# Optimization experiments

Measured on AMD Instinct MI355X. Metric: run time of the kernel, lower is better.

## Reference

```python
import jax, jax.numpy as jnp
import numpy as np

N = 100000
E = 1600000
IN_DIM, HID_DIM, OUT_DIM = 128, 64, 32


def setup_inputs() -> dict:
    key = jax.random.key(0)
    k1, k2, k3, k4, k5, k6 = jax.random.split(key, 6)
    x = jax.random.normal(k1, (N, IN_DIM), dtype=jnp.float32)
    edge_index = jax.random.randint(k2, (2, E), 0, N, dtype=jnp.int64)
    # Glorot-ish init for GCN weights
    W1 = jax.random.normal(k3, (IN_DIM, HID_DIM), dtype=jnp.float32) / np.sqrt(IN_DIM)
    b1 = jnp.zeros((HID_DIM,), dtype=jnp.float32)
    W2 = jax.random.normal(k4, (HID_DIM, OUT_DIM), dtype=jnp.float32) / np.sqrt(HID_DIM)
    b2 = jnp.zeros((OUT_DIM,), dtype=jnp.float32)
    return {"x": x, "edge_index": edge_index, "W1": W1, "b1": b1, "W2": W2, "b2": b2}


def _gcn_norm(edge_index, num_nodes):
    # add self loops, compute symmetric normalization coefficients
    loop = jnp.arange(num_nodes, dtype=edge_index.dtype)
    row = jnp.concatenate([edge_index[0], loop])  # source
    col = jnp.concatenate([edge_index[1], loop])  # target
    deg = jax.ops.segment_sum(jnp.ones_like(col, dtype=jnp.float32), col,
                              num_segments=num_nodes)
    dinv = jax.lax.rsqrt(deg)  # deg >= 1 due to self loops
    norm = dinv[row] * dinv[col]  # [E+N]
    return row, col, norm


def _gcn_conv(x, W, b, row, col, norm, num_nodes):
    h = x @ W                       # [N, out]
    msg = h[row] * norm[:, None]    # gather + scale  [E+N, out]
    out = jax.ops.segment_sum(msg, col, num_segments=num_nodes)  # scatter-add
    return out + b


def reference(x, edge_index, W1, b1, W2, b2):
    num_nodes = x.shape[0]
    row, col, norm = _gcn_norm(edge_index, num_nodes)
    h = _gcn_conv(x, W1, b1, row, col, norm, num_nodes)
    h = jax.nn.relu(h)
    # dropout(p=0.6) is identity in eval mode
    out = _gcn_conv(h, W2, b2, row, col, norm, num_nodes)
    return out
```

## Files before the change

### kernel.cpp

```cpp
#include <hip/hip_runtime.h>
#include <hip/hip_fp16.h>


#define NNODES 100000
#define NEDGES 1600000
#define IN_DIM 128
#define HID 64
#define OUTD 32

#define BKT_NODES 128
#define NBUK 782
#define BKT_CAP 3584
#define P1_BLOCKS 256
#define P1_CHUNK (NEDGES / P1_BLOCKS)


__global__ __launch_bounds__(256) void k_pass1(const int* __restrict__ row,
                                               const int* __restrict__ col,
                                               int* __restrict__ gcur,
                                               unsigned int* __restrict__ pairbuf) {
    __shared__ int lcnt[NBUK];
    __shared__ int lbase[NBUK];
    int t = threadIdx.x;
    int e0 = blockIdx.x * P1_CHUNK;
    int e1 = e0 + P1_CHUNK;
    for (int j = t; j < NBUK; j += 256) lcnt[j] = 0;
    __syncthreads();
    for (int e = e0 + t; e < e1; e += 256)
        atomicAdd(&lcnt[col[e] >> 7], 1);
    __syncthreads();
    for (int j = t; j < NBUK; j += 256) {
        int n = lcnt[j];
        lbase[j] = (n > 0) ? atomicAdd(&gcur[j], n) : 0;
    }
    __syncthreads();
    for (int j = t; j < NBUK; j += 256) lcnt[j] = 0;
    __syncthreads();
    for (int e = e0 + t; e < e1; e += 256) {
        int c = col[e];
        unsigned int pk = ((unsigned int)row[e] << 7) | (unsigned int)(c & 127);
        int b = c >> 7;
        int pos = lbase[b] + atomicAdd(&lcnt[b], 1);
        if (pos < BKT_CAP) pairbuf[(size_t)b * BKT_CAP + pos] = pk;
    }
}

__global__ __launch_bounds__(256) void k_pass2(const unsigned int* __restrict__ pairbuf,
                                               const int* __restrict__ gcur,
                                               int* __restrict__ ptr,
                                               float* __restrict__ dinv,
                                               int* __restrict__ adj) {
    __shared__ int ncnt[BKT_NODES];
    __shared__ int nsc[BKT_NODES];
    __shared__ int ncur[BKT_NODES];
    __shared__ int red[256];
    __shared__ int seg[BKT_CAP];
    int b = blockIdx.x;
    int t = threadIdx.x;

    int part = 0;
    for (int j = t; j < b; j += 256) part += gcur[j];
    red[t] = part;
    __syncthreads();
    for (int o = 128; o > 0; o >>= 1) {
        if (t < o) red[t] += red[t + o];
        __syncthreads();
    }
    int base = red[0];

    int c0 = b * BKT_NODES;
    int nb = NNODES - c0; if (nb > BKT_NODES) nb = BKT_NODES;
    int size = gcur[b]; if (size > BKT_CAP) size = BKT_CAP;
    const unsigned int* pp = pairbuf + (size_t)b * BKT_CAP;

    if (t < BKT_NODES) ncnt[t] = 0;
    __syncthreads();
    for (int k = t; k < size; k += 256)
        atomicAdd(&ncnt[pp[k] & 127u], 1);
    __syncthreads();
    int myv = (t < BKT_NODES) ? ncnt[t] : 0;
    if (t < BKT_NODES) nsc[t] = myv;
    __syncthreads();
    for (int off = 1; off < BKT_NODES; off <<= 1) {
        int u = 0;
        if (t < BKT_NODES && t >= off) u = nsc[t - off];
        __syncthreads();
        if (t < BKT_NODES) nsc[t] += u;
        __syncthreads();
    }
    if (t < BKT_NODES) {
        int excl = nsc[t] - myv;
        ncur[t] = excl;
        if (t < nb) {
            ptr[c0 + t] = base + excl;
            dinv[c0 + t] = rsqrtf((float)myv + 1.0f);
        }
    }
    if (b == NBUK - 1 && t == 0) ptr[NNODES] = NEDGES;
    __syncthreads();
    for (int k = t; k < size; k += 256) {
        unsigned int pk = pp[k];
        int pos = atomicAdd(&ncur[pk & 127u], 1);
        seg[pos] = (int)(pk >> 7);
    }
    __syncthreads();
    for (int k = t; k < size; k += 256) adj[base + k] = seg[k];
}


#define TILE 64
#define NT 16
__global__ __launch_bounds__(256) void k_gemm1(const float* __restrict__ x,
                                               const float* __restrict__ W1,
                                               const float* __restrict__ dinv,
                                               __half* __restrict__ g1) {
    __shared__ float shx[TILE][IN_DIM];
    int t = threadIdx.x;
    int nbase = blockIdx.x * TILE;

    const float4* xg = reinterpret_cast<const float4*>(x + (size_t)nbase * IN_DIM);
    float4* shx4 = reinterpret_cast<float4*>(&shx[0][0]);
    int lim = (NNODES - nbase) * (IN_DIM / 4);
    if (lim > TILE * (IN_DIM / 4)) lim = TILE * (IN_DIM / 4);
#pragma unroll
    for (int it = 0; it < 8; ++it) {
        int idx = t + it * 256;
        if (idx < lim) shx4[idx] = xg[idx];
    }
    __syncthreads();

    int w = t >> 6;
    int lane = t & 63;
    int n0 = w * NT;

    float acc[NT];
#pragma unroll
    for (int n = 0; n < NT; ++n) acc[n] = 0.0f;

    for (int kc = 0; kc < IN_DIM / 4; ++kc) {
        float w0 = W1[(kc * 4 + 0) * HID + lane];
        float w1 = W1[(kc * 4 + 1) * HID + lane];
        float w2 = W1[(kc * 4 + 2) * HID + lane];
        float w3 = W1[(kc * 4 + 3) * HID + lane];
#pragma unroll
        for (int n = 0; n < NT; ++n) {
            float4 xv = *reinterpret_cast<const float4*>(&shx[n0 + n][kc * 4]);
            acc[n] = fmaf(xv.x, w0, acc[n]);
            acc[n] = fmaf(xv.y, w1, acc[n]);
            acc[n] = fmaf(xv.z, w2, acc[n]);
            acc[n] = fmaf(xv.w, w3, acc[n]);
        }
    }
#pragma unroll
    for (int n = 0; n < NT; ++n) {
        int node = nbase + n0 + n;
        if (node < NNODES)
            g1[(unsigned)node * HID + lane] = __float2half(dinv[node] * acc[n]);
    }
}

__global__ __launch_bounds__(256) void k_agg1g2(const uint2* __restrict__ g1q,
                                                const int* __restrict__ ptr,
                                                const int* __restrict__ adj,
                                                const float* __restrict__ dinv,
                                                const float* __restrict__ b1,
                                                const float* __restrict__ W2,
                                                __half* __restrict__ g2,
                                                int ibase) {
    __shared__ float sh[4][HID];
    int t = blockIdx.x * blockDim.x + threadIdx.x;
    int i = ibase + (t >> 6);
    if (i >= NNODES) return;
    unsigned lane = threadIdx.x & 63;
    int w = threadIdx.x >> 6;
    unsigned q  = lane >> 4;
    unsigned hl = lane & 15;

    float4 acc = make_float4(0.f, 0.f, 0.f, 0.f);
    auto addrow = [&](unsigned n) {
        uint2 v = g1q[(n << 4) + hl];
        float2 fa = __half22float2(*reinterpret_cast<const __half2*>(&v.x));
        float2 fb = __half22float2(*reinterpret_cast<const __half2*>(&v.y));
        acc.x += fa.x; acc.y += fa.y; acc.z += fb.x; acc.w += fb.y;
    };

    if (q == 0) addrow((unsigned)i);
    int p0 = ptr[i], p1 = ptr[i + 1];
    int p = p0;
    for (; p + 16 <= p1; p += 16) {
        int n0 = adj[p + q];
        int n1 = adj[p + 4 + q];
        int n2 = adj[p + 8 + q];
        int n3 = adj[p + 12 + q];
        addrow((unsigned)n0);
        addrow((unsigned)n1);
        addrow((unsigned)n2);
        addrow((unsigned)n3);
    }
    for (; p + 4 <= p1; p += 4) {
        int n = adj[p + q];
        addrow((unsigned)n);
    }
    int rem = p1 - p;
    if ((int)q < rem) {
        int n = adj[p + q];
        addrow((unsigned)n);
    }
    acc.x += __shfl_xor(acc.x, 16); acc.y += __shfl_xor(acc.y, 16);
    acc.z += __shfl_xor(acc.z, 16); acc.w += __shfl_xor(acc.w, 16);
    acc.x += __shfl_xor(acc.x, 32); acc.y += __shfl_xor(acc.y, 32);
    acc.z += __shfl_xor(acc.z, 32); acc.w += __shfl_xor(acc.w, 32);

    float di = dinv[i];
    if (q == 0) {
        float4 bb = reinterpret_cast<const float4*>(b1)[hl];
        float4 h;
        h.x = fmaxf(fmaf(di, acc.x, bb.x), 0.f);
        h.y = fmaxf(fmaf(di, acc.y, bb.y), 0.f);
        h.z = fmaxf(fmaf(di, acc.z, bb.z), 0.f);
        h.w = fmaxf(fmaf(di, acc.w, bb.w), 0.f);
        *reinterpret_cast<float4*>(&sh[w][4 * hl]) = h;
    }

    unsigned j2 = lane & 31;
    unsigned half = lane >> 5;
    float mv = 0.0f;
#pragma unroll
    for (int j = 0; j < 32; ++j) {
        unsigned jj = half * 32 + j;
        mv = fmaf(sh[w][jj], W2[jj * OUTD + j2], mv);
    }
    mv += __shfl_xor(mv, 32);
    if (half == 0) g2[((unsigned)i << 5) + j2] = __float2half(di * mv);
}

__global__ __launch_bounds__(256) void k_agg2(const uint2* __restrict__ g2q,
                                              const int* __restrict__ ptr,
                                              const int* __restrict__ adj,
                                              const float* __restrict__ dinv,
                                              const float* __restrict__ b2,
                                              float4* __restrict__ out4) {
    int t = blockIdx.x * blockDim.x + threadIdx.x;
    int i = t >> 6;
    if (i >= NNODES) return;
    unsigned lane = threadIdx.x & 63;
    unsigned q  = lane >> 3;
    unsigned hl = lane & 7;

    float4 acc = make_float4(0.f, 0.f, 0.f, 0.f);
    auto addrow = [&](unsigned n) {
        uint2 v = g2q[(n << 3) + hl];
        float2 fa = __half22float2(*reinterpret_cast<const __half2*>(&v.x));
        float2 fb = __half22float2(*reinterpret_cast<const __half2*>(&v.y));
        acc.x += fa.x; acc.y += fa.y; acc.z += fb.x; acc.w += fb.y;
    };

    if (q == 0) addrow((unsigned)i);
    int p0 = ptr[i], p1 = ptr[i + 1];
    int p = p0;
    for (; p + 16 <= p1; p += 16) {
        int n0 = adj[p + q];
        int n1 = adj[p + 8 + q];
        addrow((unsigned)n0);
        addrow((unsigned)n1);
    }
    for (; p + 8 <= p1; p += 8) {
        int n = adj[p + q];
        addrow((unsigned)n);
    }
    int rem = p1 - p;
    if ((int)q < rem) {
        int n = adj[p + q];
        addrow((unsigned)n);
    }
    acc.x += __shfl_xor(acc.x, 8);  acc.y += __shfl_xor(acc.y, 8);
    acc.z += __shfl_xor(acc.z, 8);  acc.w += __shfl_xor(acc.w, 8);
    acc.x += __shfl_xor(acc.x, 16); acc.y += __shfl_xor(acc.y, 16);
    acc.z += __shfl_xor(acc.z, 16); acc.w += __shfl_xor(acc.w, 16);
    acc.x += __shfl_xor(acc.x, 32); acc.y += __shfl_xor(acc.y, 32);
    acc.z += __shfl_xor(acc.z, 32); acc.w += __shfl_xor(acc.w, 32);

    if (q == 0) {
        float di = dinv[i];
        float4 bb = reinterpret_cast<const float4*>(b2)[hl];
        out4[((unsigned)i << 3) + hl] =
            make_float4(fmaf(di, acc.x, bb.x), fmaf(di, acc.y, bb.y),
                        fmaf(di, acc.z, bb.z), fmaf(di, acc.w, bb.w));
    }
}

extern "C" void kernel_launch(void* const* d_in, const int* in_sizes, int n_in,
                              void* d_out, int out_size, void* d_ws, size_t ws_size,
                              hipStream_t stream) {
    const float* x  = (const float*)d_in[0];
    const int*   ei = (const int*)d_in[1];
    const float* W1 = (const float*)d_in[2];
    const float* b1 = (const float*)d_in[3];
    const float* W2 = (const float*)d_in[4];
    const float* b2 = (const float*)d_in[5];
    float4* out = (float4*)d_out;

    const int* row = ei;
    const int* col = ei + NEDGES;

    char* ws = (char*)d_ws;
    size_t off = 0;
    auto alloc = [&](size_t bytes) {
        void* p = ws + off;
        off = (off + bytes + 511) & ~(size_t)511;
        return p;
    };
    int*    gcur = (int*)   alloc((size_t)NBUK * 4);
    int*    ptr  = (int*)   alloc((size_t)(NNODES + 1) * 4);
    float*  dinv = (float*) alloc((size_t)NNODES * 4);
    int*    adj  = (int*)   alloc((size_t)NEDGES * 4);
    __half* g2   = (__half*)alloc((size_t)NNODES * OUTD * 2);
    size_t big = (size_t)NBUK * BKT_CAP * 4;
    size_t g1b = (size_t)NNODES * HID * 2;
    unsigned int* pairbuf = (unsigned int*)alloc(big > g1b ? big : g1b);
    __half* g1 = (__half*)pairbuf;

    const int B = 256;
    hipMemsetAsync(gcur, 0, (size_t)NBUK * 4, stream);
    k_pass1<<<P1_BLOCKS, 256, 0, stream>>>(row, col, gcur, pairbuf);
    k_pass2<<<NBUK, 256, 0, stream>>>(pairbuf, gcur, ptr, dinv, adj);

    {
        int nblk = (NNODES + TILE - 1) / TILE;
        k_gemm1<<<nblk, 256, 0, stream>>>(x, W1, dinv, g1);
    }
    {
        const int H0 = 50048;
        int nblk0 = H0 / 4;
        int nblk1 = (NNODES - H0 + 3) / 4;
        k_agg1g2<<<nblk0, B, 0, stream>>>(
            (const uint2*)g1, ptr, adj, dinv, b1, W2, g2, 0);
        k_agg1g2<<<nblk1, B, 0, stream>>>(
            (const uint2*)g1, ptr, adj, dinv, b1, W2, g2, H0);
    }
    {
        long long tot = (long long)NNODES * 64;
        k_agg2<<<(int)((tot + B - 1) / B), B, 0, stream>>>(
            (const uint2*)g2, ptr, adj, dinv, b2, out);
    }
}
```

Before: 286.9 us.

## Use fp16 MFMA for first GEMM and merge split aggregation launches

Replaces the fp32 FMA shared-memory GEMM for x@W1 with per-wave 16x16x32 fp16 MFMA instructions. A new one-block kernel pre-converts W1 to fp16 in MFMA fragment layout, and x rows are converted to fp16 in registers. The two half-range launches of the layer-1 aggregation are merged into a single launch. This lowers GEMM compute cost and launch overhead, but reduces the precision of the x@W1 inputs to fp16.

```diff
diff --git a/kernel.cpp b/kernel.cpp
--- a/kernel.cpp
+++ b/kernel.cpp
@@ -13,6 +13,9 @@
 #define BKT_CAP 3584
 #define P1_BLOCKS 256
 #define P1_CHUNK (NEDGES / P1_BLOCKS)
+
+typedef _Float16 f16x8 __attribute__((ext_vector_type(8)));
+typedef float f32x4 __attribute__((ext_vector_type(4)));
 
 
 __global__ __launch_bounds__(256) void k_pass1(const int* __restrict__ row,
@@ -108,54 +111,63 @@
 }
 
 
-#define TILE 64
-#define NT 16
+__global__ __launch_bounds__(256) void k_cvtW(const float* __restrict__ W1,
+                                              _Float16* __restrict__ W1h) {
+    int t = threadIdx.x;
+#pragma unroll
+    for (int it = 0; it < 4; ++it) {
+        int fl = t + it * 256;
+        int slot = fl >> 6;
+        int l = fl & 63;
+        int kk = slot >> 2, nt = slot & 3;
+        int kbase = kk * 32 + ((l >> 4) << 3);
+        int n = nt * 16 + (l & 15);
+        _Float16* dst = W1h + (size_t)fl * 8;
+#pragma unroll
+        for (int j = 0; j < 8; ++j)
+            dst[j] = (_Float16)W1[(kbase + j) * HID + n];
+    }
+}
+
 __global__ __launch_bounds__(256) void k_gemm1(const float* __restrict__ x,
-                                               const float* __restrict__ W1,
+                                               const f16x8* __restrict__ W1h,
                                                const float* __restrict__ dinv,
                                                __half* __restrict__ g1) {
-    __shared__ float shx[TILE][IN_DIM];
-    int t = threadIdx.x;
-    int nbase = blockIdx.x * TILE;
-
-    const float4* xg = reinterpret_cast<const float4*>(x + (size_t)nbase * IN_DIM);
-    float4* shx4 = reinterpret_cast<float4*>(&shx[0][0]);
-    int lim = (NNODES - nbase) * (IN_DIM / 4);
-    if (lim > TILE * (IN_DIM / 4)) lim = TILE * (IN_DIM / 4);
-#pragma unroll
-    for (int it = 0; it < 8; ++it) {
-        int idx = t + it * 256;
-        if (idx < lim) shx4[idx] = xg[idx];
-    }
-    __syncthreads();
-
-    int w = t >> 6;
-    int lane = t & 63;
-    int n0 = w * NT;
-
-    float acc[NT];
-#pragma unroll
-    for (int n = 0; n < NT; ++n) acc[n] = 0.0f;
-
-    for (int kc = 0; kc < IN_DIM / 4; ++kc) {
-        float w0 = W1[(kc * 4 + 0) * HID + lane];
-        float w1 = W1[(kc * 4 + 1) * HID + lane];
-        float w2 = W1[(kc * 4 + 2) * HID + lane];
-        float w3 = W1[(kc * 4 + 3) * HID + lane];
-#pragma unroll
-        for (int n = 0; n < NT; ++n) {
-            float4 xv = *reinterpret_cast<const float4*>(&shx[n0 + n][kc * 4]);
-            acc[n] = fmaf(xv.x, w0, acc[n]);
-            acc[n] = fmaf(xv.y, w1, acc[n]);
-            acc[n] = fmaf(xv.z, w2, acc[n]);
-            acc[n] = fmaf(xv.w, w3, acc[n]);
-        }
-    }
-#pragma unroll
-    for (int n = 0; n < NT; ++n) {
-        int node = nbase + n0 + n;
-        if (node < NNODES)
-            g1[(unsigned)node * HID + lane] = __float2half(dinv[node] * acc[n]);
+    int w = threadIdx.x >> 6;
+    int l = threadIdx.x & 63;
+    int nbase = blockIdx.x * 64 + w * 16;
+    if (nbase >= NNODES) return;
+
+    f16x8 bf[16];
+#pragma unroll
+    for (int s = 0; s < 16; ++s) bf[s] = W1h[s * 64 + l];
+
+    f32x4 acc[4] = {};
+    const float* xrow = x + (size_t)(nbase + (l & 15)) * IN_DIM + ((l >> 4) << 3);
+#pragma unroll
+    for (int kk = 0; kk < 4; ++kk) {
+        float4 a0 = *reinterpret_cast<const float4*>(xrow + kk * 32);
+        float4 a1 = *reinterpret_cast<const float4*>(xrow + kk * 32 + 4);
+        f16x8 af;
+        af[0] = (_Float16)a0.x; af[1] = (_Float16)a0.y;
+        af[2] = (_Float16)a0.z; af[3] = (_Float16)a0.w;
+        af[4] = (_Float16)a1.x; af[5] = (_Float16)a1.y;
+        af[6] = (_Float16)a1.z; af[7] = (_Float16)a1.w;
+#pragma unroll
+        for (int nt = 0; nt < 4; ++nt)
+            acc[nt] = __builtin_amdgcn_mfma_f32_16x16x32_f16(af, bf[kk * 4 + nt],
+                                                             acc[nt], 0, 0, 0);
+    }
+    int rbase = nbase + ((l >> 4) << 2);
+    float dv[4];
+#pragma unroll
+    for (int r = 0; r < 4; ++r) dv[r] = dinv[rbase + r];
+#pragma unroll
+    for (int nt = 0; nt < 4; ++nt) {
+        int feat = nt * 16 + (l & 15);
+#pragma unroll
+        for (int r = 0; r < 4; ++r)
+            g1[(size_t)(rbase + r) * HID + feat] = __float2half(dv[r] * acc[nt][r]);
     }
 }
 
@@ -165,11 +177,10 @@
                                                 const float* __restrict__ dinv,
                                                 const float* __restrict__ b1,
                                                 const float* __restrict__ W2,
-                                                __half* __restrict__ g2,
-                                                int ibase) {
+                                                __half* __restrict__ g2) {
     __shared__ float sh[4][HID];
     int t = blockIdx.x * blockDim.x + threadIdx.x;
-    int i = ibase + (t >> 6);
+    int i = t >> 6;
     if (i >= NNODES) return;
     unsigned lane = threadIdx.x & 63;
     int w = threadIdx.x >> 6;
@@ -310,11 +321,12 @@
         off = (off + bytes + 511) & ~(size_t)511;
         return p;
     };
-    int*    gcur = (int*)   alloc((size_t)NBUK * 4);
-    int*    ptr  = (int*)   alloc((size_t)(NNODES + 1) * 4);
-    float*  dinv = (float*) alloc((size_t)NNODES * 4);
-    int*    adj  = (int*)   alloc((size_t)NEDGES * 4);
-    __half* g2   = (__half*)alloc((size_t)NNODES * OUTD * 2);
+    int*       gcur = (int*)      alloc((size_t)NBUK * 4);
+    int*       ptr  = (int*)      alloc((size_t)(NNODES + 1) * 4);
+    float*     dinv = (float*)    alloc((size_t)NNODES * 4);
+    int*       adj  = (int*)      alloc((size_t)NEDGES * 4);
+    __half*    g2   = (__half*)   alloc((size_t)NNODES * OUTD * 2);
+    _Float16*  W1h  = (_Float16*) alloc((size_t)IN_DIM * HID * 2);
     size_t big = (size_t)NBUK * BKT_CAP * 4;
     size_t g1b = (size_t)NNODES * HID * 2;
     unsigned int* pairbuf = (unsigned int*)alloc(big > g1b ? big : g1b);
@@ -322,21 +334,18 @@
 
     const int B = 256;
     hipMemsetAsync(gcur, 0, (size_t)NBUK * 4, stream);
+    k_cvtW<<<1, 256, 0, stream>>>(W1, W1h);
     k_pass1<<<P1_BLOCKS, 256, 0, stream>>>(row, col, gcur, pairbuf);
     k_pass2<<<NBUK, 256, 0, stream>>>(pairbuf, gcur, ptr, dinv, adj);
 
     {
-        int nblk = (NNODES + TILE - 1) / TILE;
-        k_gemm1<<<nblk, 256, 0, stream>>>(x, W1, dinv, g1);
+        int nblk = (NNODES + 63) / 64;
+        k_gemm1<<<nblk, 256, 0, stream>>>(x, (const f16x8*)W1h, dinv, g1);
     }
     {
-        const int H0 = 50048;
-        int nblk0 = H0 / 4;
-        int nblk1 = (NNODES - H0 + 3) / 4;
-        k_agg1g2<<<nblk0, B, 0, stream>>>(
-            (const uint2*)g1, ptr, adj, dinv, b1, W2, g2, 0);
-        k_agg1g2<<<nblk1, B, 0, stream>>>(
-            (const uint2*)g1, ptr, adj, dinv, b1, W2, g2, H0);
+        long long tot = (long long)NNODES * 64;
+        k_agg1g2<<<(int)((tot + B - 1) / B), B, 0, stream>>>(
+            (const uint2*)g1, ptr, adj, dinv, b1, W2, g2);
     }
     {
         long long tot = (long long)NNODES * 64;
```

New measurement: 257.0 us. 10.4% less time.
